# Kernel optimization log

Hardware: AMD Instinct MI355X
Metric: run time of the kernel (lower is better)

## Reference

```python
import jax, jax.numpy as jnp
import numpy as np

N, M, K = 4, 50, 240000
POS_THRESH = 0.7
NEG_THRESH = 0.3
RPN_BATCH = 512
NUM_FG = RPN_BATCH // 2
NUM_BG = RPN_BATCH - NUM_FG
NEG_INF = -1e9


def setup_inputs() -> dict:
    key = jax.random.key(0)
    k1, k2, k3, k4, k5, k6 = jax.random.split(key, 6)
    # anchors: valid boxes (x1,y1,x2,y2) inside a ~960x600 image
    a_xy = jax.random.uniform(k1, (K, 2)) * jnp.array([900.0, 550.0])
    a_wh = jax.random.uniform(k2, (K, 2)) * 120.0 + 16.0
    anchors = jnp.concatenate([a_xy, a_xy + a_wh], axis=-1)
    g_xy = jax.random.uniform(k3, (N, M, 2)) * jnp.array([900.0, 550.0])
    g_wh = jax.random.uniform(k4, (N, M, 2)) * 120.0 + 16.0
    gt_boxes = jnp.concatenate([g_xy, g_xy + g_wh], axis=-1)
    rpn_cls_score = jax.random.normal(k5, (N, K))
    gt_labels = jax.random.randint(k6, (N, M), 1, 3, dtype=jnp.int32)
    return {"anchors": anchors, "rpn_cls_score": rpn_cls_score,
            "gt_boxes": gt_boxes, "gt_labels": gt_labels}


def _iou(anchors, gt_boxes):
    # anchors (K,4), gt_boxes (N,M,4) -> (N,K,M)
    a = anchors[None, :, None, :]   # (1,K,1,4)
    g = gt_boxes[:, None, :, :]     # (N,1,M,4)
    lt = jnp.maximum(a[..., :2], g[..., :2])
    rb = jnp.minimum(a[..., 2:], g[..., 2:])
    wh = jnp.clip(rb - lt, 0.0)
    inter = wh[..., 0] * wh[..., 1]
    area_a = (a[..., 2] - a[..., 0]) * (a[..., 3] - a[..., 1])
    area_g = (g[..., 2] - g[..., 0]) * (g[..., 3] - g[..., 1])
    return inter / (area_a + area_g - inter + 1e-8)


def _encode(anchors, matched):
    # anchors (K,4), matched (N,K,4) -> (N,K,4) standard (dx,dy,dw,dh)
    aw = anchors[:, 2] - anchors[:, 0]
    ah = anchors[:, 3] - anchors[:, 1]
    acx = anchors[:, 0] + 0.5 * aw
    acy = anchors[:, 1] + 0.5 * ah
    gw = matched[..., 2] - matched[..., 0]
    gh = matched[..., 3] - matched[..., 1]
    gcx = matched[..., 0] + 0.5 * gw
    gcy = matched[..., 1] + 0.5 * gh
    return jnp.stack([(gcx - acx) / aw, (gcy - acy) / ah,
                      jnp.log(gw / aw), jnp.log(gh / ah)], axis=-1)


def _subsample_one(score, pos, neg):
    # deterministic balanced sampler: top NUM_FG positives and top NUM_BG
    # negatives ranked by objectness criterion (hard mining)
    pos_key = jnp.where(pos, score, NEG_INF)
    neg_key = jnp.where(neg, score, NEG_INF)
    pv, pi = jax.lax.top_k(pos_key, NUM_FG)
    nv, ni = jax.lax.top_k(neg_key, NUM_BG)
    mask = jnp.zeros(score.shape[0], dtype=score.dtype)
    mask = mask.at[pi].max((pv > NEG_INF / 2).astype(score.dtype))
    mask = mask.at[ni].max((nv > NEG_INF / 2).astype(score.dtype))
    return mask


def reference(anchors, rpn_cls_score, gt_boxes, gt_labels):
    ious = _iou(anchors, gt_boxes)                 # (N,K,M)
    max_o = jnp.max(ious, axis=-1)                 # (N,K)
    argm = jnp.argmax(ious, axis=-1)               # (N,K)
    pos = max_o >= POS_THRESH
    neg = max_o < NEG_THRESH
    matched = jnp.take_along_axis(
        gt_boxes, jnp.broadcast_to(argm[:, :, None], (N, K, 4)), axis=1)
    matched_labels = jnp.take_along_axis(gt_labels, argm, axis=1)
    cls_targets = jnp.where(pos, matched_labels, 0)
    reg_targets = _encode(anchors, matched) * pos[..., None].astype(anchors.dtype)
    cls_weights = (pos | neg).astype(anchors.dtype)
    reg_weights = pos.astype(anchors.dtype)
    mask = jax.vmap(_subsample_one)(rpn_cls_score, pos, neg)  # (N,K)
    cls_weights = cls_weights * mask
    reg_weights = reg_weights * mask
    return cls_targets, reg_targets, cls_weights, reg_weights
```

## Files before the change

kernel.cpp:

```cpp
#include <hip/hip_runtime.h>

#define KA 240000
#define NI 4
#define MG 50
#define NSEL 256u
#define CAPL 4096
#define BPI 235
#define GRID (BPI * NI)

typedef unsigned int u32;

#define METAO 16384
#define LISTO (METAO + 32)
#define ONE_F 0x3F800000u

static __device__ __forceinline__ u32 sortkey32(float f) {
    u32 b = __float_as_uint(f);
    return (b & 0x80000000u) ? ~b : (b | 0x80000000u);
}
static __device__ __forceinline__ void patch1(u32* p) {
    __hip_atomic_store(p, ONE_F, __ATOMIC_RELAXED, __HIP_MEMORY_SCOPE_AGENT);
}

extern "C" __global__ void __launch_bounds__(256, 4)
AnchorTargetLayer_48052094107725_kernel(
    const float4* __restrict__ anchors, const float* __restrict__ scores,
    const float4* __restrict__ gtb, const int* __restrict__ glab,
    float* __restrict__ out, u32* __restrict__ flags, u32* __restrict__ ws) {
#pragma clang fp contract(off)
    __shared__ float4 gA[MG];
    __shared__ int glb[MG];
    __shared__ u32 lh[2048];
    const int bx = blockIdx.x;
    const int tid = threadIdx.x;
    const int n = bx / BPI;
    const int kb = bx - n * BPI;

    if (tid < 18) {
        const int i = bx * 18 + tid;
        if (i < LISTO) atomicExch(&ws[i], 0u);
    }
    for (int i = tid; i < 2048; i += 256) lh[i] = 0;
    if (tid < MG) {
        gA[tid] = gtb[n * MG + tid];
        glb[tid] = glab[n * MG + tid];
    }
    __syncthreads();

    const int k0 = (kb * 256 + tid) * 4;
    if (k0 < KA) {
        float ax0[4], ay0[4], ax2[4], ay2[4];
        #pragma unroll
        for (int j = 0; j < 4; ++j) {
            const float4 A = anchors[k0 + j];
            ax0[j] = A.x; ay0[j] = A.y; ax2[j] = A.z; ay2[j] = A.w;
        }
        float aaw[4], aah[4], aar[4], bst[4];
        int bix[4];
        #pragma unroll
        for (int j = 0; j < 4; ++j) {
            aaw[j] = ax2[j] - ax0[j];
            aah[j] = ay2[j] - ay0[j];
            aar[j] = aaw[j] * aah[j];
            bst[j] = -1.0f;
            bix[j] = 0;
        }
        for (int m = 0; m < MG; m += 2) {
            const float4 Ga = gA[m];
            const float4 Gb = gA[m + 1];
            const float gaA = (Ga.z - Ga.x) * (Ga.w - Ga.y);
            const float gaB = (Gb.z - Gb.x) * (Gb.w - Gb.y);
            #pragma unroll
            for (int j = 0; j < 4; ++j) {
                const float wa = fmaxf(fminf(ax2[j], Ga.z) - fmaxf(ax0[j], Ga.x), 0.0f);
                const float ha = fmaxf(fminf(ay2[j], Ga.w) - fmaxf(ay0[j], Ga.y), 0.0f);
                const float ia = wa * ha;
                const float qa = ia / (((aar[j] + gaA) - ia) + 1e-8f);
                const float wb = fmaxf(fminf(ax2[j], Gb.z) - fmaxf(ax0[j], Gb.x), 0.0f);
                const float hb = fmaxf(fminf(ay2[j], Gb.w) - fmaxf(ay0[j], Gb.y), 0.0f);
                const float ib = wb * hb;
                const float qb = ib / (((aar[j] + gaB) - ib) + 1e-8f);
                if (qa > bst[j]) { bst[j] = qa; bix[j] = m; }
                if (qb > bst[j]) { bst[j] = qb; bix[j] = m + 1; }
            }
        }

        const int nk = n * KA + k0;
        const float4 s4 = ((const float4*)scores)[nk >> 2];
        const float scv[4] = {s4.x, s4.y, s4.z, s4.w};

        float clsv[4];
        float4 regv[4];
        u32 flagpack = 0;
        #pragma unroll
        for (int j = 0; j < 4; ++j) {
            const bool pos = bst[j] >= 0.7f;
            const bool neg = bst[j] < 0.3f;
            clsv[j] = pos ? (float)glb[bix[j]] : 0.0f;
            float4 rv = make_float4(0.0f, 0.0f, 0.0f, 0.0f);
            if (pos) {
                const float4 Gm = gA[bix[j]];
                const float gw = Gm.z - Gm.x, gh = Gm.w - Gm.y;
                const float gcx = Gm.x + 0.5f * gw, gcy = Gm.y + 0.5f * gh;
                const float acx = ax0[j] + 0.5f * aaw[j], acy = ay0[j] + 0.5f * aah[j];
                rv.x = (gcx - acx) / aaw[j];
                rv.y = (gcy - acy) / aah[j];
                rv.z = logf(gw / aaw[j]);
                rv.w = logf(gh / aah[j]);
            }
            regv[j] = rv;
            const u32 fl = pos ? 1u : (neg ? 2u : 0u);
            flagpack |= fl << (8 * j);
            if (fl) atomicAdd(&lh[sortkey32(scv[j]) >> 21], fl == 2u ? 0x10000u : 1u);
        }
        const size_t NK = (size_t)NI * KA;
        const size_t NK4 = NK / 4;
        const int t4 = nk >> 2;
        ((float4*)out)[t4] = make_float4(clsv[0], clsv[1], clsv[2], clsv[3]);
        float4* regp = ((float4*)(out + NK)) + nk;
        regp[0] = regv[0]; regp[1] = regv[1]; regp[2] = regv[2]; regp[3] = regv[3];
        const float4 z4 = make_float4(0.0f, 0.0f, 0.0f, 0.0f);
        ((float4*)out)[5 * NK4 + t4] = z4;
        ((float4*)out)[6 * NK4 + t4] = z4;
        flags[t4] = flagpack;
    }
    __syncthreads();
    const int gp = 2 * n;
    for (int i = tid; i < 2048; i += 256) {
        const u32 c = lh[i];
        if (c & 0xFFFFu) atomicAdd(&ws[gp * 2048 + i], c & 0xFFFFu);
        if (c >> 16)     atomicAdd(&ws[(gp + 1) * 2048 + i], c >> 16);
    }
}

__global__ void __launch_bounds__(256) kP(const float* __restrict__ scores,
                                          const u32* __restrict__ flagsW,
                                          u32* __restrict__ ws,
                                          float* __restrict__ out) {
    __shared__ u32 cs[256];
    __shared__ u32 s_us[2], s_R[2], s_done[2];
    const int bx = blockIdx.x, tid = threadIdx.x;
    const int n = bx / BPI, kb = bx - n * BPI;
    u32* hist = ws;
    u32* meta = ws + METAO;
    u32* list = ws + LISTO;

    for (int gi = 0; gi < 2; ++gi) {
        const int g = 2 * n + gi;
        u32 loc[8];
        u32 s = 0;
        const int base = g * 2048 + tid * 8;
        #pragma unroll
        for (int j = 0; j < 8; ++j) { loc[j] = hist[base + j]; s += loc[j]; }
        cs[tid] = s;
        __syncthreads();
        for (int d = 1; d < 256; d <<= 1) {
            const u32 add = (tid + d < 256) ? cs[tid + d] : 0u;
            __syncthreads();
            cs[tid] += add;
            __syncthreads();
        }
        if (tid == 0) s_done[gi] = (cs[0] < NSEL) ? 1u : 0u;
        u32 run = (tid < 255) ? cs[tid + 1] : 0u;
        #pragma unroll
        for (int j = 7; j >= 0; --j) {
            const u32 Sj = run + loc[j];
            if (Sj >= NSEL && run < NSEL) {
                s_us[gi] = (u32)(tid * 8 + j);
                s_R[gi] = NSEL - run;
            }
            run = Sj;
        }
        __syncthreads();
    }
    if (kb == 0 && tid == 0) {
        meta[2 * n] = s_us[0];     meta[8 + 2 * n] = s_R[0];     meta[16 + 2 * n] = s_done[0];
        meta[2 * n + 1] = s_us[1]; meta[8 + 2 * n + 1] = s_R[1]; meta[16 + 2 * n + 1] = s_done[1];
    }

    const int k0 = (kb * 256 + tid) * 4;
    if (k0 >= KA) return;
    const int nk = n * KA + k0;
    const u32 fw = flagsW[nk >> 2];
    if (!fw) return;
    const float4 s4 = ((const float4*)scores)[nk >> 2];
    const float scv[4] = {s4.x, s4.y, s4.z, s4.w};
    const size_t NK = (size_t)NI * KA;
    u32* o32 = (u32*)out;
    #pragma unroll
    for (int j = 0; j < 4; ++j) {
        const u32 f = (fw >> (8 * j)) & 255u;
        if (!f) continue;
        const int gi = (f == 2u) ? 1 : 0;
        bool in = false;
        if (s_done[gi]) {
            in = true;
        } else {
            const u32 key = sortkey32(scv[j]);
            const u32 p11 = key >> 21;
            if (p11 > s_us[gi]) {
                in = true;
            } else if (p11 == s_us[gi]) {
                const int g = 2 * n + gi;
                const u32 p = atomicAdd(&meta[24 + g], 1u);
                if (p < CAPL) {
                    list[(g * CAPL + p) * 2] = key;
                    list[(g * CAPL + p) * 2 + 1] = (u32)(k0 + j);
                }
            }
        }
        if (in) {
            patch1(&o32[5 * NK + nk + j]);
            if (f == 1u) patch1(&o32[6 * NK + nk + j]);
        }
    }
}

__global__ void __launch_bounds__(256) kR2(const u32* __restrict__ ws,
                                           float* __restrict__ out) {
    __shared__ u32 h2[1024];
    __shared__ u32 cs[256];
    __shared__ u32 s_usb, s_R2, s_tc;
    __shared__ u32 tk[256], ti[256];
    const u32* meta = ws + METAO;
    const u32* list = ws + LISTO;
    const int g = blockIdx.x, tid = threadIdx.x;
    if (meta[16 + g]) return;
    u32 c = meta[24 + g];
    if (c > CAPL) c = CAPL;
    const u32 R1 = meta[8 + g];
    for (u32 i = tid; i < 1024; i += 256) h2[i] = 0;
    if (tid == 0) s_tc = 0;
    __syncthreads();
    for (u32 j = tid; j < c; j += 256)
        atomicAdd(&h2[(list[(g * CAPL + j) * 2] >> 11) & 1023u], 1u);
    __syncthreads();
    u32 loc[4];
    u32 s = 0;
    #pragma unroll
    for (int j = 0; j < 4; ++j) { loc[j] = h2[tid * 4 + j]; s += loc[j]; }
    cs[tid] = s;
    __syncthreads();
    for (int d = 1; d < 256; d <<= 1) {
        const u32 add = (tid + d < 256) ? cs[tid + d] : 0u;
        __syncthreads();
        cs[tid] += add;
        __syncthreads();
    }
    u32 run = (tid < 255) ? cs[tid + 1] : 0u;
    #pragma unroll
    for (int j = 3; j >= 0; --j) {
        const u32 Sj = run + loc[j];
        if (Sj >= R1 && run < R1) { s_usb = (u32)(tid * 4 + j); s_R2 = R1 - run; }
        run = Sj;
    }
    __syncthreads();
    const u32 usb = s_usb, R2 = s_R2;
    const int nn = g >> 1;
    const bool posg = ((g & 1) == 0);
    const size_t NK = (size_t)NI * KA;
    u32* o32 = (u32*)out;
    for (u32 j = tid; j < c; j += 256) {
        const u32 key = list[(g * CAPL + j) * 2];
        const u32 idx = list[(g * CAPL + j) * 2 + 1];
        const u32 sb = (key >> 11) & 1023u;
        if (sb > usb) {
            const size_t o = (size_t)nn * KA + idx;
            patch1(&o32[5 * NK + o]);
            if (posg) patch1(&o32[6 * NK + o]);
        } else if (sb == usb) {
            const u32 p = atomicAdd(&s_tc, 1u);
            if (p < 256) { tk[p] = key; ti[p] = idx; }
        }
    }
    __syncthreads();
    u32 tc = s_tc;
    if (tc > 256) tc = 256;
    for (u32 i = tid; i < tc; i += 256) {
        const u32 ki = tk[i], ii = ti[i];
        u32 rank = 0;
        for (u32 j = 0; j < tc; ++j) {
            const u32 kj = tk[j];
            if (kj > ki || (kj == ki && ti[j] < ii)) rank++;
        }
        if (rank < R2) {
            const size_t o = (size_t)nn * KA + ii;
            patch1(&o32[5 * NK + o]);
            if (posg) patch1(&o32[6 * NK + o]);
        }
    }
}

extern "C" void kernel_launch(void* const* d_in, const int* in_sizes, int n_in,
                              void* d_out, int out_size, void* d_ws, size_t ws_size,
                              hipStream_t stream) {
    (void)in_sizes; (void)n_in; (void)out_size; (void)ws_size;
    const float4* anchors = (const float4*)d_in[0];
    const float*  scores  = (const float*)d_in[1];
    const float4* gtb     = (const float4*)d_in[2];
    const int*    glab    = (const int*)d_in[3];
    float* out = (float*)d_out;

    u32* ws = (u32*)d_ws;
    u32* flags = ws + LISTO + 8 * CAPL * 2;

    AnchorTargetLayer_48052094107725_kernel<<<GRID, 256, 0, stream>>>(
        anchors, scores, gtb, glab, out, flags, ws);
    kP<<<GRID, 256, 0, stream>>>(scores, flags, ws, out);
    kR2<<<8, 256, 0, stream>>>(ws, out);
}
```

Measured before the change: 137.7 us.

## Fuse threshold scan and refine pass into last-block-done tails, drop third kernel

The histogram prefix-scan that every kP block used to repeat now runs once per image, in the last block of the first kernel to finish, chosen through an atomic arrival counter. That block writes the threshold metadata to workspace, and kP only loads it. The second-level refine pass that lived in the separate kR2 kernel moves into the last-arriving kP block per image, which removes one launch and the redundant per-block scans. The cost is extra thread fences and atomics, plus serialized tail work in a single block per image. Arrival counters are zeroed by the first kernel, which relies on the counters being reset before they are used within the same launch.

```diff
diff --git a/kernel.cpp b/kernel.cpp
--- a/kernel.cpp
+++ b/kernel.cpp
@@ -11,7 +11,10 @@
 typedef unsigned int u32;
 
 #define METAO 16384
-#define LISTO (METAO + 32)
+#define ARR1O 16416
+#define ARR2O 16420
+#define LISTO 16424
+#define ZERON 16424
 #define ONE_F 0x3F800000u
 
 static __device__ __forceinline__ u32 sortkey32(float f) {
@@ -20,6 +23,9 @@
 }
 static __device__ __forceinline__ void patch1(u32* p) {
     __hip_atomic_store(p, ONE_F, __ATOMIC_RELAXED, __HIP_MEMORY_SCOPE_AGENT);
+}
+static __device__ __forceinline__ u32 aload(const u32* p) {
+    return __hip_atomic_load(p, __ATOMIC_RELAXED, __HIP_MEMORY_SCOPE_AGENT);
 }
 
 extern "C" __global__ void __launch_bounds__(256, 4)
@@ -38,7 +44,7 @@
 
     if (tid < 18) {
         const int i = bx * 18 + tid;
-        if (i < LISTO) atomicExch(&ws[i], 0u);
+        if (i < ZERON) atomicExch(&ws[i], 0u);
     }
     for (int i = tid; i < 2048; i += 256) lh[i] = 0;
     if (tid < MG) {
@@ -131,27 +137,132 @@
         if (c & 0xFFFFu) atomicAdd(&ws[gp * 2048 + i], c & 0xFFFFu);
         if (c >> 16)     atomicAdd(&ws[(gp + 1) * 2048 + i], c >> 16);
     }
+
+    __threadfence();
+    __syncthreads();
+    __shared__ u32 s_last;
+    if (tid == 0)
+        s_last = __hip_atomic_fetch_add(&ws[ARR1O + n], 1u,
+                                        __ATOMIC_ACQ_REL, __HIP_MEMORY_SCOPE_AGENT);
+    __syncthreads();
+    if (s_last == BPI - 1) {
+        for (int gi = 0; gi < 2; ++gi) {
+            const int g = 2 * n + gi;
+            u32 loc[8];
+            u32 s = 0;
+            const int base = g * 2048 + tid * 8;
+            #pragma unroll
+            for (int j = 0; j < 8; ++j) { loc[j] = aload(&ws[base + j]); s += loc[j]; }
+            lh[tid] = s;
+            __syncthreads();
+            for (int d = 1; d < 256; d <<= 1) {
+                const u32 add = (tid + d < 256) ? lh[tid + d] : 0u;
+                __syncthreads();
+                lh[tid] += add;
+                __syncthreads();
+            }
+            if (tid == 0)
+                ws[METAO + 16 + g] = (lh[0] < NSEL) ? 1u : 0u;
+            u32 run = (tid < 255) ? lh[tid + 1] : 0u;
+            #pragma unroll
+            for (int j = 7; j >= 0; --j) {
+                const u32 Sj = run + loc[j];
+                if (Sj >= NSEL && run < NSEL) {
+                    ws[METAO + g] = (u32)(tid * 8 + j);
+                    ws[METAO + 8 + g] = NSEL - run;
+                }
+                run = Sj;
+            }
+            __syncthreads();
+        }
+    }
 }
 
 __global__ void __launch_bounds__(256) kP(const float* __restrict__ scores,
                                           const u32* __restrict__ flagsW,
                                           u32* __restrict__ ws,
                                           float* __restrict__ out) {
-    __shared__ u32 cs[256];
-    __shared__ u32 s_us[2], s_R[2], s_done[2];
+    __shared__ u32 s_us[2], s_done[2];
     const int bx = blockIdx.x, tid = threadIdx.x;
     const int n = bx / BPI, kb = bx - n * BPI;
-    u32* hist = ws;
     u32* meta = ws + METAO;
     u32* list = ws + LISTO;
 
+    if (tid < 2) {
+        s_us[tid]   = meta[2 * n + tid];
+        s_done[tid] = meta[16 + 2 * n + tid];
+    }
+    __syncthreads();
+
+    const size_t NK = (size_t)NI * KA;
+    u32* o32 = (u32*)out;
+
+    const int k0 = (kb * 256 + tid) * 4;
+    if (k0 < KA) {
+        const int nk = n * KA + k0;
+        const u32 fw = flagsW[nk >> 2];
+        if (fw) {
+            const float4 s4 = ((const float4*)scores)[nk >> 2];
+            const float scv[4] = {s4.x, s4.y, s4.z, s4.w};
+            #pragma unroll
+            for (int j = 0; j < 4; ++j) {
+                const u32 f = (fw >> (8 * j)) & 255u;
+                if (!f) continue;
+                const int gi = (f == 2u) ? 1 : 0;
+                bool in = false;
+                if (s_done[gi]) {
+                    in = true;
+                } else {
+                    const u32 key = sortkey32(scv[j]);
+                    const u32 p11 = key >> 21;
+                    if (p11 > s_us[gi]) {
+                        in = true;
+                    } else if (p11 == s_us[gi]) {
+                        const int g = 2 * n + gi;
+                        const u32 p = atomicAdd(&meta[24 + g], 1u);
+                        if (p < CAPL) {
+                            list[(g * CAPL + p) * 2] = key;
+                            list[(g * CAPL + p) * 2 + 1] = (u32)(k0 + j);
+                        }
+                    }
+                }
+                if (in) {
+                    patch1(&o32[5 * NK + nk + j]);
+                    if (f == 1u) patch1(&o32[6 * NK + nk + j]);
+                }
+            }
+        }
+    }
+
+    __threadfence();
+    __syncthreads();
+    __shared__ u32 s_last;
+    if (tid == 0)
+        s_last = __hip_atomic_fetch_add(&ws[ARR2O + n], 1u,
+                                        __ATOMIC_ACQ_REL, __HIP_MEMORY_SCOPE_AGENT);
+    __syncthreads();
+    if (s_last != BPI - 1) return;
+
+    __shared__ u32 h2[1024];
+    __shared__ u32 cs[256];
+    __shared__ u32 s_usb, s_R2, s_tc;
+    __shared__ u32 tk[256], ti[256];
     for (int gi = 0; gi < 2; ++gi) {
+        if (s_done[gi]) continue;
         const int g = 2 * n + gi;
-        u32 loc[8];
+        u32 c = aload(&meta[24 + g]);
+        if (c > CAPL) c = CAPL;
+        const u32 R1 = meta[8 + g];
+        for (u32 i = tid; i < 1024; i += 256) h2[i] = 0;
+        if (tid == 0) s_tc = 0;
+        __syncthreads();
+        for (u32 j = tid; j < c; j += 256)
+            atomicAdd(&h2[(aload(&list[(g * CAPL + j) * 2]) >> 11) & 1023u], 1u);
+        __syncthreads();
+        u32 loc[4];
         u32 s = 0;
-        const int base = g * 2048 + tid * 8;
-        #pragma unroll
-        for (int j = 0; j < 8; ++j) { loc[j] = hist[base + j]; s += loc[j]; }
+        #pragma unroll
+        for (int j = 0; j < 4; ++j) { loc[j] = h2[tid * 4 + j]; s += loc[j]; }
         cs[tid] = s;
         __syncthreads();
         for (int d = 1; d < 256; d <<= 1) {
@@ -160,134 +271,46 @@
             cs[tid] += add;
             __syncthreads();
         }
-        if (tid == 0) s_done[gi] = (cs[0] < NSEL) ? 1u : 0u;
         u32 run = (tid < 255) ? cs[tid + 1] : 0u;
         #pragma unroll
-        for (int j = 7; j >= 0; --j) {
+        for (int j = 3; j >= 0; --j) {
             const u32 Sj = run + loc[j];
-            if (Sj >= NSEL && run < NSEL) {
-                s_us[gi] = (u32)(tid * 8 + j);
-                s_R[gi] = NSEL - run;
-            }
+            if (Sj >= R1 && run < R1) { s_usb = (u32)(tid * 4 + j); s_R2 = R1 - run; }
             run = Sj;
         }
         __syncthreads();
-    }
-    if (kb == 0 && tid == 0) {
-        meta[2 * n] = s_us[0];     meta[8 + 2 * n] = s_R[0];     meta[16 + 2 * n] = s_done[0];
-        meta[2 * n + 1] = s_us[1]; meta[8 + 2 * n + 1] = s_R[1]; meta[16 + 2 * n + 1] = s_done[1];
-    }
-
-    const int k0 = (kb * 256 + tid) * 4;
-    if (k0 >= KA) return;
-    const int nk = n * KA + k0;
-    const u32 fw = flagsW[nk >> 2];
-    if (!fw) return;
-    const float4 s4 = ((const float4*)scores)[nk >> 2];
-    const float scv[4] = {s4.x, s4.y, s4.z, s4.w};
-    const size_t NK = (size_t)NI * KA;
-    u32* o32 = (u32*)out;
-    #pragma unroll
-    for (int j = 0; j < 4; ++j) {
-        const u32 f = (fw >> (8 * j)) & 255u;
-        if (!f) continue;
-        const int gi = (f == 2u) ? 1 : 0;
-        bool in = false;
-        if (s_done[gi]) {
-            in = true;
-        } else {
-            const u32 key = sortkey32(scv[j]);
-            const u32 p11 = key >> 21;
-            if (p11 > s_us[gi]) {
-                in = true;
-            } else if (p11 == s_us[gi]) {
-                const int g = 2 * n + gi;
-                const u32 p = atomicAdd(&meta[24 + g], 1u);
-                if (p < CAPL) {
-                    list[(g * CAPL + p) * 2] = key;
-                    list[(g * CAPL + p) * 2 + 1] = (u32)(k0 + j);
-                }
-            }
-        }
-        if (in) {
-            patch1(&o32[5 * NK + nk + j]);
-            if (f == 1u) patch1(&o32[6 * NK + nk + j]);
-        }
-    }
-}
-
-__global__ void __launch_bounds__(256) kR2(const u32* __restrict__ ws,
-                                           float* __restrict__ out) {
-    __shared__ u32 h2[1024];
-    __shared__ u32 cs[256];
-    __shared__ u32 s_usb, s_R2, s_tc;
-    __shared__ u32 tk[256], ti[256];
-    const u32* meta = ws + METAO;
-    const u32* list = ws + LISTO;
-    const int g = blockIdx.x, tid = threadIdx.x;
-    if (meta[16 + g]) return;
-    u32 c = meta[24 + g];
-    if (c > CAPL) c = CAPL;
-    const u32 R1 = meta[8 + g];
-    for (u32 i = tid; i < 1024; i += 256) h2[i] = 0;
-    if (tid == 0) s_tc = 0;
-    __syncthreads();
-    for (u32 j = tid; j < c; j += 256)
-        atomicAdd(&h2[(list[(g * CAPL + j) * 2] >> 11) & 1023u], 1u);
-    __syncthreads();
-    u32 loc[4];
-    u32 s = 0;
-    #pragma unroll
-    for (int j = 0; j < 4; ++j) { loc[j] = h2[tid * 4 + j]; s += loc[j]; }
-    cs[tid] = s;
-    __syncthreads();
-    for (int d = 1; d < 256; d <<= 1) {
-        const u32 add = (tid + d < 256) ? cs[tid + d] : 0u;
-        __syncthreads();
-        cs[tid] += add;
-        __syncthreads();
-    }
-    u32 run = (tid < 255) ? cs[tid + 1] : 0u;
-    #pragma unroll
-    for (int j = 3; j >= 0; --j) {
-        const u32 Sj = run + loc[j];
-        if (Sj >= R1 && run < R1) { s_usb = (u32)(tid * 4 + j); s_R2 = R1 - run; }
-        run = Sj;
-    }
-    __syncthreads();
-    const u32 usb = s_usb, R2 = s_R2;
-    const int nn = g >> 1;
-    const bool posg = ((g & 1) == 0);
-    const size_t NK = (size_t)NI * KA;
-    u32* o32 = (u32*)out;
-    for (u32 j = tid; j < c; j += 256) {
-        const u32 key = list[(g * CAPL + j) * 2];
-        const u32 idx = list[(g * CAPL + j) * 2 + 1];
-        const u32 sb = (key >> 11) & 1023u;
-        if (sb > usb) {
-            const size_t o = (size_t)nn * KA + idx;
-            patch1(&o32[5 * NK + o]);
-            if (posg) patch1(&o32[6 * NK + o]);
-        } else if (sb == usb) {
-            const u32 p = atomicAdd(&s_tc, 1u);
-            if (p < 256) { tk[p] = key; ti[p] = idx; }
-        }
-    }
-    __syncthreads();
-    u32 tc = s_tc;
-    if (tc > 256) tc = 256;
-    for (u32 i = tid; i < tc; i += 256) {
-        const u32 ki = tk[i], ii = ti[i];
-        u32 rank = 0;
-        for (u32 j = 0; j < tc; ++j) {
-            const u32 kj = tk[j];
-            if (kj > ki || (kj == ki && ti[j] < ii)) rank++;
-        }
-        if (rank < R2) {
-            const size_t o = (size_t)nn * KA + ii;
-            patch1(&o32[5 * NK + o]);
-            if (posg) patch1(&o32[6 * NK + o]);
-        }
+        const u32 usb = s_usb, R2 = s_R2;
+        const bool posg = (gi == 0);
+        for (u32 j = tid; j < c; j += 256) {
+            const u32 key = aload(&list[(g * CAPL + j) * 2]);
+            const u32 idx = aload(&list[(g * CAPL + j) * 2 + 1]);
+            const u32 sb = (key >> 11) & 1023u;
+            if (sb > usb) {
+                const size_t o = (size_t)n * KA + idx;
+                patch1(&o32[5 * NK + o]);
+                if (posg) patch1(&o32[6 * NK + o]);
+            } else if (sb == usb) {
+                const u32 p = atomicAdd(&s_tc, 1u);
+                if (p < 256) { tk[p] = key; ti[p] = idx; }
+            }
+        }
+        __syncthreads();
+        u32 tc = s_tc;
+        if (tc > 256) tc = 256;
+        for (u32 i = tid; i < tc; i += 256) {
+            const u32 ki = tk[i], ii = ti[i];
+            u32 rank = 0;
+            for (u32 j2 = 0; j2 < tc; ++j2) {
+                const u32 kj = tk[j2];
+                if (kj > ki || (kj == ki && ti[j2] < ii)) rank++;
+            }
+            if (rank < R2) {
+                const size_t o = (size_t)n * KA + ii;
+                patch1(&o32[5 * NK + o]);
+                if (posg) patch1(&o32[6 * NK + o]);
+            }
+        }
+        __syncthreads();
     }
 }
 
@@ -307,5 +330,4 @@
     AnchorTargetLayer_48052094107725_kernel<<<GRID, 256, 0, stream>>>(
         anchors, scores, gtb, glab, out, flags, ws);
     kP<<<GRID, 256, 0, stream>>>(scores, flags, ws, out);
-    kR2<<<8, 256, 0, stream>>>(ws, out);
-}
+}
```

Measured after the change: 324.0 us. +135.4%, slower.
